# Optimization experiments

Measured on AMD Instinct MI355X. Metric: run time of the kernel, lower is better.

## Reference

```python
import jax, jax.numpy as jnp
import numpy as np

RX = (2, 9)
RY = (4, 9)
G, O = 64, 2          # column chunk size and overlap (hardcoded in original forward)
GK = RX[1]            # Gaussian (uniform box) kernel size, must be odd
M = N = 512


def _patches(x, kh, kw, pc, pr):
    # torch: F.pad(x,(pr,pr,pc,pc)).unfold(-2,kh,1).unfold(-2,kw,1).flatten(-2)
    xp = jnp.pad(x, ((0, 0), (0, 0), (pc, pc), (pr, pr)))
    p = jax.lax.conv_general_dilated_patches(xp, (kh, kw), (1, 1), 'VALID')  # (b, kh*kw, m, n) since c==1
    return jnp.moveaxis(p, 1, -1)[:, None]  # (b,1,m,n,kh*kw)


def _spatial_kernel(kh, kw):
    d = (jnp.arange(kh, dtype=jnp.float32) - kh // 2)[:, None] ** 2 \
        + (jnp.arange(kw, dtype=jnp.float32) - kw // 2)[None, :] ** 2
    return jnp.exp(-d.reshape(-1) / ((kh * kw) / 4.0) ** 2)


def _gen_weight(ych, kh, kw, pc, pr, sigma):
    p = _patches(ych, kh, kw, pc, pr)
    w = jnp.exp(-((p - ych[..., None]) ** 2) / (sigma / 2.0) ** 2)  # range (bilateral) term
    w = w * _spatial_kernel(kh, kw)                                  # spatial Gaussian term
    w = w * _patches(jnp.ones_like(ych), kh, kw, pc, pr)             # zero out padded taps
    return w / w.sum(-1, keepdims=True)


def _boxfilter(x, weight, kh, kw, pc, pr):
    return (_patches(x, kh, kw, pc, pr) * weight).sum(-1)


def _forward(X, y, r):
    sigma = r[0] * (y.max() - y.min())
    kh0, kw0, pc0, pr0 = 2 * RX[0] + 1, 2 * RY[0] + 1, RX[0], RY[0]  # detail kernel
    kh1, kw1, pc1, pr1 = 2 * RX[1] + 1, 2 * RY[1] + 1, RX[1], RY[1]  # base kernel
    gk = jnp.ones((1, 1, GK, GK), X.dtype) / float(GK * GK)
    pad = GK // 2
    conv = lambda z: jax.lax.conv_general_dilated(z, gk, (1, 1), [(pad, pad), (pad, pad)])

    # Angle = [0]: rotate(.,0,expand=True) and CenterCrop(m,n) are identities.
    XX, yy = X, y
    XXbase, yybase = conv(XX), conv(yy)
    XXdetail, yydetail = XX - XXbase, yy - yybase

    n = X.shape[-1]
    idx = np.arange(n)
    chunks = [idx[i:i + G] for i in range(0, n, G - O)]
    if len(chunks[-1]) <= 5:
        chunks[-2] = np.arange(chunks[-2][0], n)
        del chunks[-1]

    bdetail, Abase, bbase = [], [], []
    for index, ck in enumerate(chunks):
        s, e = int(ck[0]), int(ck[-1]) + 1
        Xb, Xd = XXbase[..., s:e], XXdetail[..., s:e]
        yb, yd = yybase[..., s:e], yydetail[..., s:e]
        wD = _gen_weight(Xd, kh0, kw0, pc0, pr0, sigma)
        wB = _gen_weight(Xb, kh1, kw1, pc1, pr1, sigma)
        lo = 0 if index == 0 else O // 2
        hi = None if index == len(chunks) - 1 else -(O // 2)
        bdetail.append(_boxfilter(yd - Xd, wD, kh0, kw0, pc0, pr0)[..., lo:hi])
        mean_y = _boxfilter(yb, wB, kh1, kw1, pc1, pr1)
        mean_x = _boxfilter(Xb, wB, kh1, kw1, pc1, pr1)
        var_x = _boxfilter(Xb * Xb, wB, kh1, kw1, pc1, pr1) - mean_x * mean_x
        cov_xy = _boxfilter(Xb * yb, wB, kh1, kw1, pc1, pr1) - mean_x * mean_y
        A = cov_xy / (var_x + 1e-6)
        b = mean_y - A * mean_x
        bbase.append(b[..., lo:hi])
        Abase.append(A[..., lo:hi])

    bdetail = jnp.concatenate(bdetail, -1)
    Abase = jnp.concatenate(Abase, -1)
    bbase = jnp.concatenate(bbase, -1)
    return Abase * XXbase + bbase + XXdetail + bdetail


def setup_inputs() -> dict:
    key = jax.random.key(0)
    k1, k2, k3 = jax.random.split(key, 3)
    X = jax.random.uniform(k1, (1, 1, M, N), dtype=jnp.float32)
    y = jax.random.uniform(k2, (1, 1, M, N), dtype=jnp.float32)
    r = jax.random.uniform(k3, (1,), dtype=jnp.float32)
    return {"X": X, "y": y, "r": r}


def reference(X, y, r):
    return _forward(X, y, r)
```

## Files before the change

kernel.cpp:

```cpp
#include <hip/hip_runtime.h>

#define W 512

typedef float v2f __attribute__((ext_vector_type(2)));

__device__ __forceinline__ float fexp2(float x) {
#if __has_builtin(__builtin_amdgcn_exp2f)
    return __builtin_amdgcn_exp2f(x);
#else
    return __expf(x * 0.6931471805599453f);
#endif
}
__device__ __forceinline__ v2f vfma(v2f a, v2f b, v2f c) {
    return __builtin_elementwise_fma(a, b, c);
}
__device__ __forceinline__ v2f bc2(float x) { v2f r; r.x = x; r.y = x; return r; }

__global__ __launch_bounds__(256) void k_minmax(const float* __restrict__ y,
                                                float2* __restrict__ partial) {
    __shared__ float smn[256], smx[256];
    int t = threadIdx.x;
    const float4* y4 = (const float4*)y;
    float4 v = y4[blockIdx.x * 256 + t];
    float mn = fminf(fminf(v.x, v.y), fminf(v.z, v.w));
    float mx = fmaxf(fmaxf(v.x, v.y), fmaxf(v.z, v.w));
    smn[t] = mn; smx[t] = mx;
    __syncthreads();
    for (int off = 128; off > 0; off >>= 1) {
        if (t < off) {
            smn[t] = fminf(smn[t], smn[t + off]);
            smx[t] = fmaxf(smx[t], smx[t + off]);
        }
        __syncthreads();
    }
    if (t == 0) partial[blockIdx.x] = make_float2(smn[0], smx[0]);
}

__global__ __launch_bounds__(256) void k_fused(const float* __restrict__ X,
                                               const float* __restrict__ y,
                                               const float2* __restrict__ partial,
                                               const float* __restrict__ r,
                                               float* __restrict__ out) {
    __shared__ float sbx[19];
    __shared__ float sdy[5];
    __shared__ __align__(16) char ldsbuf[60256];
    float*  sX  = (float*)ldsbuf;
    float*  sY  = sX + 34 * 90;
    float*  csX = sY + 34 * 90;
    float*  csY = csX + 26 * 90;
    float2* bXY = (float2*)(csY + 26 * 90);
    float2* dXD = (float2*)csX;
    float2* red = (float2*)sX;

    int tx = threadIdx.x, ty = threadIdx.y;
    int t = ty * 64 + tx;
    int c0 = blockIdx.x * 64, r0 = blockIdx.y * 8;

    if (t < 19)      { int d = t - 9;      sbx[t]      = __expf(-(float)(d * d) / 8145.0625f); }
    else if (t < 24) { int d = t - 19 - 2; sdy[t - 19] = __expf(-(float)(d * d) / 126.5625f); }

    red[t] = partial[t];
    __syncthreads();
    for (int off = 128; off > 0; off >>= 1) {
        if (t < off) {
            red[t].x = fminf(red[t].x, red[t + off].x);
            red[t].y = fmaxf(red[t].y, red[t + off].y);
        }
        __syncthreads();
    }
    float2 mm0 = red[0];
    __syncthreads();
    float sigma = r[0] * (mm0.y - mm0.x);
    float hh = 0.5f * sigma;
    float k2 = -1.4426950408889634f / (hh * hh);
    v2f k2v = bc2(k2);

    for (int i = t; i < 34 * 90; i += 256) {
        int rr = i / 90, cc2 = i - rr * 90;
        int gr = r0 - 13 + rr, gc = c0 - 13 + cc2;
        bool ok = ((unsigned)gr < 512u) & ((unsigned)gc < 512u);
        float xv = 0.f, yv = 0.f;
        if (ok) { xv = X[gr * W + gc]; yv = y[gr * W + gc]; }
        sX[i] = xv; sY[i] = yv;
    }
    __syncthreads();

    for (int i = t; i < 26 * 90; i += 256) {
        int rr = i / 90, cc2 = i - rr * 90;
        float ax = 0.f, ay = 0.f;
#pragma unroll
        for (int k = 0; k < 9; ++k) { ax += sX[(rr + k) * 90 + cc2]; ay += sY[(rr + k) * 90 + cc2]; }
        csX[i] = ax; csY[i] = ay;
    }
    __syncthreads();

    const float inv81 = 1.0f / 81.0f;
    for (int i = t; i < 26 * 82; i += 256) {
        int rr = i / 82, cc2 = i - rr * 82;
        float ax = 0.f, ay = 0.f;
#pragma unroll
        for (int k = 0; k < 9; ++k) { ax += csX[rr * 90 + cc2 + k]; ay += csY[rr * 90 + cc2 + k]; }
        bXY[i] = make_float2(ax * inv81, ay * inv81);
    }
    __syncthreads();

    for (int i = t; i < 12 * 72; i += 256) {
        int rr = i / 72, cc2 = i - rr * 72;
        float2 b2 = bXY[(rr + 7) * 82 + (cc2 + 5)];
        float xc = sX[(rr + 11) * 90 + (cc2 + 9)];
        float yc = sY[(rr + 11) * 90 + (cc2 + 9)];
        float xd = xc - b2.x;
        dXD[i] = make_float2(xd, (yc - b2.y) - xd);
    }
    __syncthreads();

    int c  = blockIdx.x * 64 + tx;
    int h0 = r0 + ty * 2;

    int chunk = (c == 0) ? 0 : (c - 1) / 62;
    if (chunk > 8) chunk = 8;
    int s = 62 * chunk;
    int e = (chunk == 8) ? 512 : (s + 64);

    const float ksb = -1.4426950408889634f / 8145.0625f;
    const float ksd = -1.4426950408889634f / 126.5625f;
    float cc[19];
#pragma unroll
    for (int j = 0; j < 19; ++j) {
        int nc = c - 9 + j, d = j - 9;
        cc[j] = ((nc >= s) & (nc < e)) ? ksb * (float)(d * d) : -1e30f;
    }
    float ccd[9];
#pragma unroll
    for (int j = 0; j < 9; ++j) {
        int nc = c - 4 + j, d = j - 4;
        ccd[j] = ((nc >= s) & (nc < e)) ? ksd * (float)(d * d) : -1e30f;
    }

    v2f Xc2; Xc2.x = bXY[(2 * ty + 9)  * 82 + tx + 9].x;
             Xc2.y = bXY[(2 * ty + 10) * 82 + tx + 9].x;
    v2f Xd2; Xd2.x = dXD[(2 * ty + 2) * 72 + tx + 4].x;
             Xd2.y = dXD[(2 * ty + 3) * 72 + tx + 4].x;

    v2f sw = bc2(0.f), swx = bc2(0.f), swy = bc2(0.f), swxx = bc2(0.f), swxy = bc2(0.f);
#pragma unroll 1
    for (int nh = h0 - 9; nh <= h0 + 10; ++nh) {
        if ((unsigned)nh >= 512u) continue;
        int dy0 = nh - h0;
        const float2* xr = bXY + (nh - r0 + 9) * 82 + tx;
        v2f rs = bc2(0.f), rsx = bc2(0.f), rsy = bc2(0.f), rsxx = bc2(0.f), rsxy = bc2(0.f);
#pragma unroll
        for (int j = 0; j < 19; ++j) {
            float2 v = xr[j];
            v2f xv = bc2(v.x), yv = bc2(v.y);
            v2f u = xv - Xc2;
            v2f a = vfma(u * k2v, u, bc2(cc[j]));
            v2f w; w.x = fexp2(a.x); w.y = fexp2(a.y);
            rs = rs + w;
            rsx = vfma(w, xv, rsx);
            rsy = vfma(w, yv, rsy);
            v2f tt = w * xv;
            rsxx = vfma(tt, xv, rsxx);
            rsxy = vfma(tt, yv, rsxy);
        }
        v2f ey;
        ey.x = (dy0 <= 9)  ? sbx[dy0 + 9] : 0.f;
        ey.y = (dy0 >= -8) ? sbx[dy0 + 8] : 0.f;
        sw   = vfma(ey, rs,   sw);
        swx  = vfma(ey, rsx,  swx);
        swy  = vfma(ey, rsy,  swy);
        swxx = vfma(ey, rsxx, swxx);
        swxy = vfma(ey, rsxy, swxy);
    }

    v2f swd = bc2(0.f), sv = bc2(0.f);
#pragma unroll 1
    for (int nh = h0 - 2; nh <= h0 + 3; ++nh) {
        if ((unsigned)nh >= 512u) continue;
        int dyd = nh - h0;
        const float2* dr2 = dXD + (nh - r0 + 2) * 72 + tx;
        v2f rs = bc2(0.f), rv = bc2(0.f);
#pragma unroll
        for (int j = 0; j < 9; ++j) {
            float2 v = dr2[j];
            v2f xd = bc2(v.x), dv = bc2(v.y);
            v2f u = xd - Xd2;
            v2f a = vfma(u * k2v, u, bc2(ccd[j]));
            v2f w; w.x = fexp2(a.x); w.y = fexp2(a.y);
            rs = rs + w;
            rv = vfma(w, dv, rv);
        }
        v2f ey;
        ey.x = (dyd <= 2)  ? sdy[dyd + 2] : 0.f;
        ey.y = (dyd >= -1) ? sdy[dyd + 1] : 0.f;
        swd = vfma(ey, rs, swd);
        sv  = vfma(ey, rv, sv);
    }

    v2f inv; inv.x = 1.0f / sw.x; inv.y = 1.0f / sw.y;
    v2f mx = swx * inv, my = swy * inv;
    v2f varx = vfma(-mx, mx, swxx * inv);
    v2f cov  = vfma(-mx, my, swxy * inv);
    v2f A; A.x = cov.x / (varx.x + 1e-6f); A.y = cov.y / (varx.y + 1e-6f);
    v2f b = my - A * mx;
    v2f bd; bd.x = sv.x / swd.x; bd.y = sv.y / swd.y;
    v2f res = A * Xc2 + b + Xd2 + bd;
    int p0 = h0 * W + c;
    out[p0]     = res.x;
    out[p0 + W] = res.y;
}

extern "C" void kernel_launch(void* const* d_in, const int* in_sizes, int n_in,
                              void* d_out, int out_size, void* d_ws, size_t ws_size,
                              hipStream_t stream) {
    const float* X = (const float*)d_in[0];
    const float* y = (const float*)d_in[1];
    const float* r = (const float*)d_in[2];
    float* out = (float*)d_out;
    float2* partial = (float2*)d_ws;

    k_minmax<<<256, 256, 0, stream>>>(y, partial);
    k_fused<<<dim3(8, 64), dim3(64, 4), 0, stream>>>(X, y, partial, r, out);
}
```

Measured before the change: 92.45 us.

## Retile fused bilateral kernel to 16x16 blocks with one pixel per thread

The fused kernel moves from 64x8 tiles with two rows per thread, using packed float2 math, to square 16x16 tiles with one output pixel per thread. LDS use falls from about 60 KB to about 38 KB per block, and launch bounds now ask for 4 blocks per CU to raise occupancy. The price is a larger halo: the 26-pixel border is a bigger share of a 42x42 staging tile, so per block there is more redundant halo loading and box-filtering. The vertical reuse of ey weights and packed math across two rows is also lost.

```diff
diff --git a/kernel.cpp b/kernel.cpp
--- a/kernel.cpp
+++ b/kernel.cpp
@@ -1,8 +1,6 @@
 #include <hip/hip_runtime.h>
 
 #define W 512
-
-typedef float v2f __attribute__((ext_vector_type(2)));
 
 __device__ __forceinline__ float fexp2(float x) {
 #if __has_builtin(__builtin_amdgcn_exp2f)
@@ -11,10 +9,6 @@
     return __expf(x * 0.6931471805599453f);
 #endif
 }
-__device__ __forceinline__ v2f vfma(v2f a, v2f b, v2f c) {
-    return __builtin_elementwise_fma(a, b, c);
-}
-__device__ __forceinline__ v2f bc2(float x) { v2f r; r.x = x; r.y = x; return r; }
 
 __global__ __launch_bounds__(256) void k_minmax(const float* __restrict__ y,
                                                 float2* __restrict__ partial) {
@@ -36,28 +30,28 @@
     if (t == 0) partial[blockIdx.x] = make_float2(smn[0], smx[0]);
 }
 
-__global__ __launch_bounds__(256) void k_fused(const float* __restrict__ X,
-                                               const float* __restrict__ y,
-                                               const float2* __restrict__ partial,
-                                               const float* __restrict__ r,
-                                               float* __restrict__ out) {
+__global__ __launch_bounds__(256, 4) void k_fused(const float* __restrict__ X,
+                                                  const float* __restrict__ y,
+                                                  const float2* __restrict__ partial,
+                                                  const float* __restrict__ r,
+                                                  float* __restrict__ out) {
     __shared__ float sbx[19];
     __shared__ float sdy[5];
-    __shared__ __align__(16) char ldsbuf[60256];
+    __shared__ __align__(16) char ldsbuf[38624];
     float*  sX  = (float*)ldsbuf;
-    float*  sY  = sX + 34 * 90;
-    float*  csX = sY + 34 * 90;
-    float*  csY = csX + 26 * 90;
-    float2* bXY = (float2*)(csY + 26 * 90);
-    float2* dXD = (float2*)csX;
+    float*  sY  = sX + 42 * 42;
+    float*  csX = sY + 42 * 42;
+    float*  csY = csX + 34 * 42;
+    float2* bXY = (float2*)(csY + 34 * 42);
+    float2* dXD = bXY + 34 * 34;
     float2* red = (float2*)sX;
 
     int tx = threadIdx.x, ty = threadIdx.y;
-    int t = ty * 64 + tx;
-    int c0 = blockIdx.x * 64, r0 = blockIdx.y * 8;
-
-    if (t < 19)      { int d = t - 9;      sbx[t]      = __expf(-(float)(d * d) / 8145.0625f); }
-    else if (t < 24) { int d = t - 19 - 2; sdy[t - 19] = __expf(-(float)(d * d) / 126.5625f); }
+    int t = ty * 16 + tx;
+    int c0 = blockIdx.x * 16, r0 = blockIdx.y * 16;
+
+    if (t < 19)      { int d = t - 9;  sbx[t]      = __expf(-(float)(d * d) / 8145.0625f); }
+    else if (t < 24) { int d = t - 21; sdy[t - 19] = __expf(-(float)(d * d) / 126.5625f); }
 
     red[t] = partial[t];
     __syncthreads();
@@ -73,10 +67,9 @@
     float sigma = r[0] * (mm0.y - mm0.x);
     float hh = 0.5f * sigma;
     float k2 = -1.4426950408889634f / (hh * hh);
-    v2f k2v = bc2(k2);
-
-    for (int i = t; i < 34 * 90; i += 256) {
-        int rr = i / 90, cc2 = i - rr * 90;
+
+    for (int i = t; i < 42 * 42; i += 256) {
+        int rr = i / 42, cc2 = i - rr * 42;
         int gr = r0 - 13 + rr, gc = c0 - 13 + cc2;
         bool ok = ((unsigned)gr < 512u) & ((unsigned)gc < 512u);
         float xv = 0.f, yv = 0.f;
@@ -85,37 +78,37 @@
     }
     __syncthreads();
 
-    for (int i = t; i < 26 * 90; i += 256) {
-        int rr = i / 90, cc2 = i - rr * 90;
+    for (int i = t; i < 34 * 42; i += 256) {
+        int rr = i / 42, cc2 = i - rr * 42;
         float ax = 0.f, ay = 0.f;
 #pragma unroll
-        for (int k = 0; k < 9; ++k) { ax += sX[(rr + k) * 90 + cc2]; ay += sY[(rr + k) * 90 + cc2]; }
+        for (int k = 0; k < 9; ++k) { ax += sX[(rr + k) * 42 + cc2]; ay += sY[(rr + k) * 42 + cc2]; }
         csX[i] = ax; csY[i] = ay;
     }
     __syncthreads();
 
     const float inv81 = 1.0f / 81.0f;
-    for (int i = t; i < 26 * 82; i += 256) {
-        int rr = i / 82, cc2 = i - rr * 82;
+    for (int i = t; i < 34 * 34; i += 256) {
+        int rr = i / 34, cc2 = i - rr * 34;
         float ax = 0.f, ay = 0.f;
 #pragma unroll
-        for (int k = 0; k < 9; ++k) { ax += csX[rr * 90 + cc2 + k]; ay += csY[rr * 90 + cc2 + k]; }
+        for (int k = 0; k < 9; ++k) { ax += csX[rr * 42 + cc2 + k]; ay += csY[rr * 42 + cc2 + k]; }
         bXY[i] = make_float2(ax * inv81, ay * inv81);
     }
     __syncthreads();
 
-    for (int i = t; i < 12 * 72; i += 256) {
-        int rr = i / 72, cc2 = i - rr * 72;
-        float2 b2 = bXY[(rr + 7) * 82 + (cc2 + 5)];
-        float xc = sX[(rr + 11) * 90 + (cc2 + 9)];
-        float yc = sY[(rr + 11) * 90 + (cc2 + 9)];
+    for (int i = t; i < 20 * 24; i += 256) {
+        int rr = i / 24, cc2 = i - rr * 24;
+        float2 b2 = bXY[(rr + 7) * 34 + (cc2 + 5)];
+        float xc = sX[(rr + 11) * 42 + (cc2 + 9)];
+        float yc = sY[(rr + 11) * 42 + (cc2 + 9)];
         float xd = xc - b2.x;
         dXD[i] = make_float2(xd, (yc - b2.y) - xd);
     }
     __syncthreads();
 
-    int c  = blockIdx.x * 64 + tx;
-    int h0 = r0 + ty * 2;
+    int c = c0 + tx;
+    int h = r0 + ty;
 
     int chunk = (c == 0) ? 0 : (c - 1) / 62;
     if (chunk > 8) chunk = 8;
@@ -137,77 +130,65 @@
         ccd[j] = ((nc >= s) & (nc < e)) ? ksd * (float)(d * d) : -1e30f;
     }
 
-    v2f Xc2; Xc2.x = bXY[(2 * ty + 9)  * 82 + tx + 9].x;
-             Xc2.y = bXY[(2 * ty + 10) * 82 + tx + 9].x;
-    v2f Xd2; Xd2.x = dXD[(2 * ty + 2) * 72 + tx + 4].x;
-             Xd2.y = dXD[(2 * ty + 3) * 72 + tx + 4].x;
-
-    v2f sw = bc2(0.f), swx = bc2(0.f), swy = bc2(0.f), swxx = bc2(0.f), swxy = bc2(0.f);
+    float Xc = bXY[(ty + 9) * 34 + tx + 9].x;
+    float Xd = dXD[(ty + 2) * 24 + tx + 4].x;
+
+    float sw = 0.f, swx = 0.f, swy = 0.f, swxx = 0.f, swxy = 0.f;
 #pragma unroll 1
-    for (int nh = h0 - 9; nh <= h0 + 10; ++nh) {
+    for (int k = 0; k < 19; ++k) {
+        int nh = h - 9 + k;
         if ((unsigned)nh >= 512u) continue;
-        int dy0 = nh - h0;
-        const float2* xr = bXY + (nh - r0 + 9) * 82 + tx;
-        v2f rs = bc2(0.f), rsx = bc2(0.f), rsy = bc2(0.f), rsxx = bc2(0.f), rsxy = bc2(0.f);
+        const float2* xr = bXY + (ty + k) * 34 + tx;
+        float rs = 0.f, rsx = 0.f, rsy = 0.f, rsxx = 0.f, rsxy = 0.f;
 #pragma unroll
         for (int j = 0; j < 19; ++j) {
             float2 v = xr[j];
-            v2f xv = bc2(v.x), yv = bc2(v.y);
-            v2f u = xv - Xc2;
-            v2f a = vfma(u * k2v, u, bc2(cc[j]));
-            v2f w; w.x = fexp2(a.x); w.y = fexp2(a.y);
-            rs = rs + w;
-            rsx = vfma(w, xv, rsx);
-            rsy = vfma(w, yv, rsy);
-            v2f tt = w * xv;
-            rsxx = vfma(tt, xv, rsxx);
-            rsxy = vfma(tt, yv, rsxy);
-        }
-        v2f ey;
-        ey.x = (dy0 <= 9)  ? sbx[dy0 + 9] : 0.f;
-        ey.y = (dy0 >= -8) ? sbx[dy0 + 8] : 0.f;
-        sw   = vfma(ey, rs,   sw);
-        swx  = vfma(ey, rsx,  swx);
-        swy  = vfma(ey, rsy,  swy);
-        swxx = vfma(ey, rsxx, swxx);
-        swxy = vfma(ey, rsxy, swxy);
-    }
-
-    v2f swd = bc2(0.f), sv = bc2(0.f);
+            float u = v.x - Xc;
+            float a = fmaf(u * k2, u, cc[j]);
+            float w = fexp2(a);
+            rs += w;
+            rsx = fmaf(w, v.x, rsx);
+            rsy = fmaf(w, v.y, rsy);
+            float tt = w * v.x;
+            rsxx = fmaf(tt, v.x, rsxx);
+            rsxy = fmaf(tt, v.y, rsxy);
+        }
+        float ey = sbx[k];
+        sw   = fmaf(ey, rs,   sw);
+        swx  = fmaf(ey, rsx,  swx);
+        swy  = fmaf(ey, rsy,  swy);
+        swxx = fmaf(ey, rsxx, swxx);
+        swxy = fmaf(ey, rsxy, swxy);
+    }
+
+    float swd = 0.f, sv = 0.f;
 #pragma unroll 1
-    for (int nh = h0 - 2; nh <= h0 + 3; ++nh) {
+    for (int k = 0; k < 5; ++k) {
+        int nh = h - 2 + k;
         if ((unsigned)nh >= 512u) continue;
-        int dyd = nh - h0;
-        const float2* dr2 = dXD + (nh - r0 + 2) * 72 + tx;
-        v2f rs = bc2(0.f), rv = bc2(0.f);
+        const float2* dr2 = dXD + (ty + k) * 24 + tx;
+        float rs = 0.f, rv = 0.f;
 #pragma unroll
         for (int j = 0; j < 9; ++j) {
             float2 v = dr2[j];
-            v2f xd = bc2(v.x), dv = bc2(v.y);
-            v2f u = xd - Xd2;
-            v2f a = vfma(u * k2v, u, bc2(ccd[j]));
-            v2f w; w.x = fexp2(a.x); w.y = fexp2(a.y);
-            rs = rs + w;
-            rv = vfma(w, dv, rv);
-        }
-        v2f ey;
-        ey.x = (dyd <= 2)  ? sdy[dyd + 2] : 0.f;
-        ey.y = (dyd >= -1) ? sdy[dyd + 1] : 0.f;
-        swd = vfma(ey, rs, swd);
-        sv  = vfma(ey, rv, sv);
-    }
-
-    v2f inv; inv.x = 1.0f / sw.x; inv.y = 1.0f / sw.y;
-    v2f mx = swx * inv, my = swy * inv;
-    v2f varx = vfma(-mx, mx, swxx * inv);
-    v2f cov  = vfma(-mx, my, swxy * inv);
-    v2f A; A.x = cov.x / (varx.x + 1e-6f); A.y = cov.y / (varx.y + 1e-6f);
-    v2f b = my - A * mx;
-    v2f bd; bd.x = sv.x / swd.x; bd.y = sv.y / swd.y;
-    v2f res = A * Xc2 + b + Xd2 + bd;
-    int p0 = h0 * W + c;
-    out[p0]     = res.x;
-    out[p0 + W] = res.y;
+            float u = v.x - Xd;
+            float a = fmaf(u * k2, u, ccd[j]);
+            float w = fexp2(a);
+            rs += w;
+            rv = fmaf(w, v.y, rv);
+        }
+        swd = fmaf(sdy[k], rs, swd);
+        sv  = fmaf(sdy[k], rv, sv);
+    }
+
+    float inv  = 1.0f / sw;
+    float mx   = swx * inv, my = swy * inv;
+    float varx = fmaf(-mx, mx, swxx * inv);
+    float cov  = fmaf(-mx, my, swxy * inv);
+    float A    = cov / (varx + 1e-6f);
+    float b    = my - A * mx;
+    float bd   = sv / swd;
+    out[h * W + c] = fmaf(A, Xc, b) + Xd + bd;
 }
 
 extern "C" void kernel_launch(void* const* d_in, const int* in_sizes, int n_in,
@@ -220,5 +201,5 @@
     float2* partial = (float2*)d_ws;
 
     k_minmax<<<256, 256, 0, stream>>>(y, partial);
-    k_fused<<<dim3(8, 64), dim3(64, 4), 0, stream>>>(X, y, partial, r, out);
-}
+    k_fused<<<dim3(32, 32), dim3(16, 16), 0, stream>>>(X, y, partial, r, out);
+}
```

New measurement: 95.50 us. 1.03x slower.
